# Optimization experiments

Measured on AMD Instinct MI355X. Metric: run time of the kernel, lower is better.

Reference implementation:

```python
import jax, jax.numpy as jnp
import numpy as np

B, N, DX, DZ = 4, 2048, 2, 128
PPD = (128, 128)
GRID_RANGE = ((-2.0, 2.0), (-2.0, 2.0))
INIT_LS = 0.1


def _construct_grid():
    axes = [jnp.linspace(lo, hi, p, dtype=jnp.float32) for (lo, hi), p in zip(GRID_RANGE, PPD)]
    mesh = jnp.meshgrid(*axes, indexing="ij")
    return jnp.stack(mesh, axis=-1)  # [128, 128, 2]


def setup_inputs() -> dict:
    key = jax.random.key(0)
    k1, k2 = jax.random.split(key)
    x = jax.random.uniform(k1, (B, N, DX), dtype=jnp.float32, minval=-2.0, maxval=2.0)
    z = jax.random.normal(k2, (B, N, DZ), dtype=jnp.float32)
    grid = _construct_grid()
    # inverse-softplus of init lengthscale, per dim
    ls0 = jnp.full((DX,), INIT_LS, dtype=jnp.float32)
    lengthscale_param = jnp.log(jnp.exp(ls0) - 1.0)
    return {"x": x, "z": z, "grid": grid, "lengthscale_param": lengthscale_param}


def reference(x, z, grid, lengthscale_param):
    b = x.shape[0]
    grid_shape = grid.shape[:-1]  # (128, 128)
    lengthscale = 1e-05 + jax.nn.softplus(lengthscale_param)  # [dx]
    grid_flat = grid.reshape(-1, grid.shape[-1])  # [M, dx], M = 16384
    # per-dim squared distance / l^2, summed over dx  -> [b, M, n]
    diff = grid_flat[None, :, None, :] - x[:, None, :, :]  # [b, M, n, dx]
    pre_exp = jnp.sum((diff * diff) / (lengthscale ** 2), axis=-1)
    weights = jnp.exp(-0.5 * pre_exp)  # [b, M, n]
    z_grid_flat = jnp.einsum("bmn,bnd->bmd", weights, z)  # [b, M, dz]
    z_grid = z_grid_flat.reshape((b,) + grid_shape + (z.shape[-1],))
    x_grid = jnp.broadcast_to(grid[None], (b,) + grid.shape)
    return (x_grid, z_grid)
```

## Files before the change

kernel.cpp:

```cpp
#include <hip/hip_runtime.h>

#define BATCH 4
#define NPTS  2048
#define DZDIM 128
#define GD    128
#define M_TOT (GD*GD)
#define TN    32
#define PW    40
#define PZ    40
#define ZP    2112
#define WBIN  15

typedef __attribute__((ext_vector_type(8))) __bf16 bf16x8;
typedef __attribute__((ext_vector_type(4))) float floatx4;

__device__ __forceinline__ unsigned int f2bf_bits(float x){
  unsigned int u = __float_as_uint(x);
  u += 0x7FFFu + ((u >> 16) & 1u);
  return u >> 16;
}
__device__ __forceinline__ int point_bin(float px){
  int bin = __float2int_rn((px + 2.0f) * (127.0f / 4.0f));
  return min(GD - 1, max(0, bin));
}

__global__ __launch_bounds__(256) void hist_xgrid_kernel(
    const float* __restrict__ x, const float* __restrict__ grid,
    float* __restrict__ out, int* __restrict__ binStart)
{
  const int tid = threadIdx.x;
  if (blockIdx.x < BATCH){
    __shared__ int h[GD];
    __shared__ int s[GD + 1];
    const int b = blockIdx.x;
    if (tid < GD) h[tid] = 0;
    __syncthreads();
    for (int n = tid; n < NPTS; n += 256)
      atomicAdd(&h[point_bin(x[(b*NPTS + n)*2])], 1);
    __syncthreads();
    if (tid == 0){
      int acc = 0;
#pragma unroll
      for (int j = 0; j < GD; ++j){ s[j] = acc; acc += h[j]; }
      s[GD] = acc;
    }
    __syncthreads();
    if (tid <= GD) binStart[b*(GD+1) + tid] = s[tid];
  } else {
    int idx = (blockIdx.x - BATCH) * 256 + tid;
    float g = grid[idx];
#pragma unroll
    for (int b = 0; b < BATCH; ++b) out[b*(GD*GD*2) + idx] = g;
  }
}

__global__ __launch_bounds__(256) void scatter_kernel(const float* __restrict__ x,
                                                      const int* __restrict__ binStart,
                                                      float2* __restrict__ xs,
                                                      int* __restrict__ perm){
  const int b = blockIdx.y;
  const int wv = threadIdx.x >> 6, lane = threadIdx.x & 63;
  const int bin = blockIdx.x * 4 + wv;
  int base = binStart[b*(GD+1) + bin];
  const float2* __restrict__ x2 = (const float2*)x;
  for (int n0 = 0; n0 < NPTS; n0 += 64){
    int n = n0 + lane;
    float2 xv = x2[b*NPTS + n];
    bool keep = (point_bin(xv.x) == bin);
    unsigned long long mask = __ballot(keep);
    int pre = __popcll(mask & ((1ull << lane) - 1ull));
    if (keep){
      xs[(long)b*ZP + base + pre] = xv;
      perm[b*NPTS + base + pre]   = n;
    }
    base += __popcll(mask);
  }
}

__global__ __launch_bounds__(256) void ztbuild_kernel(const float* __restrict__ z,
                                                      const int* __restrict__ perm,
                                                      unsigned short* __restrict__ zt){
  const int b  = blockIdx.y;
  const int j0 = blockIdx.x * 64;
  const int jj = threadIdx.x & 63;
  const int dq = threadIdx.x >> 6;
  const int j  = j0 + jj;
  const int n  = perm[b*NPTS + j];
  const float4* __restrict__ z4 = (const float4*)z;
  const long rb = (long)(b*NPTS + n) * 32;
#pragma unroll
  for (int r = 0; r < 8; ++r){
    int c = dq*8 + r;
    float4 v = z4[rb + c];
    long o = ((long)(b*DZDIM + 4*c) * ZP) + j;
    zt[o         ] = (unsigned short)f2bf_bits(v.x);
    zt[o +   ZP  ] = (unsigned short)f2bf_bits(v.y);
    zt[o + 2*ZP  ] = (unsigned short)f2bf_bits(v.z);
    zt[o + 3*ZP  ] = (unsigned short)f2bf_bits(v.w);
  }
}

__global__ __launch_bounds__(256, 4) void setconv_mfma_kernel(
    const float2* __restrict__ xs, const int* __restrict__ binStart,
    const unsigned short* __restrict__ zt, const float* __restrict__ lsp,
    float* __restrict__ outz)
{
  __shared__ __align__(16) unsigned short Wlds[2][64 * PW];
  __shared__ __align__(16) unsigned short Zlds[2][DZDIM * PZ];

  const int tid = threadIdx.x, lane = tid & 63, wv = tid >> 6;
  const int bid = blockIdx.x;
  const int g   = bid & 7;
  const int s   = bid >> 3;
  const int h   = s & 1;
  const int b   = (s >> 1) & 3;
  const int il  = s >> 3;
  const int i   = g*16 + il;
  const int my0 = h * 64;

  const float l0 = 1e-5f + log1pf(expf(lsp[0]));
  const float l1 = 1e-5f + log1pf(expf(lsp[1]));
  const float LOG2E = 1.4426950408889634f;
  const float c0 = -0.5f * LOG2E / (l0*l0);
  const float c1 = -0.5f * LOG2E / (l1*l1);
  const float step = 4.0f / 127.0f;
  const float gx   = -2.0f + (float)i * step;

  const int lo  = binStart[b*(GD+1) + max(0, i - WBIN)];
  const int hi  = binStart[b*(GD+1) + min(GD-1, i + WBIN) + 1];
  const int lo8 = lo & ~7;
  const int len = hi - lo8;
  const int T   = (len + TN - 1) / TN;

  const int   wnp = tid & 15;
  const int   mb  = tid >> 4;
  const float gy0 = -2.0f + (float)(my0 + mb) * step;

  int goff[3];
#pragma unroll
  for (int u = 0; u < 3; ++u){
    int gi = wv + 4*u;
    if (gi < 10){
      int pos = gi*64 + lane;
      int d = pos / 5, c = pos % 5;
      if (c > 3) c = 3;
      goff[u] = (b*DZDIM + d) * ZP + c*8;
    } else goff[u] = 0;
  }

  const int q  = lane >> 4;
  const int ml = lane & 15;

  floatx4 acc[8];
#pragma unroll
  for (int tz = 0; tz < 8; ++tz) acc[tz] = (floatx4){0.f, 0.f, 0.f, 0.f};

  auto stageZ = [&](int buf, int t){
    const int k0 = lo8 + t*TN;
#pragma unroll
    for (int u = 0; u < 3; ++u){
      int gi = wv + 4*u;
      if (gi < 10){
        const unsigned short* gp = zt + goff[u] + k0;
        __builtin_amdgcn_global_load_lds(
            (__attribute__((address_space(1))) void*)gp,
            (__attribute__((address_space(3))) void*)&Zlds[buf][gi*512],
            16, 0, 0);
      }
    }
  };
  auto stageW = [&](int buf, int t){
    const int ka = t*TN + 2*wnp;
    float4 xv = *(const float4*)&xs[(long)b*ZP + lo8 + ka];
    float d0a = gx - xv.x, d0b = gx - xv.z;
    float t0a = (ka     < len) ? c0*d0a*d0a : -1.0e30f;
    float t0b = (ka + 1 < len) ? c0*d0b*d0b : -1.0e30f;
#pragma unroll
    for (int r = 0; r < 4; ++r){
      float gy  = gy0 + (float)(16*r) * step;
      float dya = gy - xv.y, dyb = gy - xv.w;
      float ua = fmaf(c1*dya, dya, t0a);
      float ub = fmaf(c1*dyb, dyb, t0b);
      unsigned int v = f2bf_bits(__builtin_amdgcn_exp2f(ua))
                     | (f2bf_bits(__builtin_amdgcn_exp2f(ub)) << 16);
      *(unsigned int*)&Wlds[buf][(mb + 16*r)*PW + 2*wnp] = v;
    }
  };
  auto domfma = [&](int buf){
    bf16x8 af = *(const bf16x8*)&Wlds[buf][(wv*16 + ml)*PW + q*8];
#pragma unroll
    for (int tz = 0; tz < 8; ++tz){
      bf16x8 bf = *(const bf16x8*)&Zlds[buf][(tz*16 + ml)*PZ + q*8];
      acc[tz] = __builtin_amdgcn_mfma_f32_16x16x32_bf16(af, bf, acc[tz], 0, 0, 0);
    }
  };

  if (T > 0){
    stageZ(0, 0);
    stageW(0, 0);
    __syncthreads();
    for (int t = 0; t < T; ++t){
      const int cur = t & 1, nxt = 1 - cur;
      if (t + 1 < T) stageZ(nxt, t + 1);
      domfma(cur);
      if (t + 1 < T) stageW(nxt, t + 1);
      __syncthreads();
    }
  }

  const long obase = ((long)(b*M_TOT + i*GD + my0 + wv*16 + q*4) << 7) + ml;
#pragma unroll
  for (int tz = 0; tz < 8; ++tz)
#pragma unroll
    for (int r = 0; r < 4; ++r)
      outz[obase + ((long)r << 7) + tz*16] = acc[tz][r];
}

extern "C" void kernel_launch(void* const* d_in, const int* in_sizes, int n_in,
                              void* d_out, int out_size, void* d_ws, size_t ws_size,
                              hipStream_t stream)
{
  const float* x    = (const float*)d_in[0];
  const float* z    = (const float*)d_in[1];
  const float* grid = (const float*)d_in[2];
  const float* lsp  = (const float*)d_in[3];
  float* out = (float*)d_out;

  char* ws = (char*)d_ws;
  int*            binStart = (int*)ws;
  int*            perm     = (int*)(ws + 2064);
  float2*         xs       = (float2*)(ws + 2064 + 32768);
  unsigned short* zt       = (unsigned short*)(ws + 2064 + 32768 + 67584);

  hipLaunchKernelGGL(hist_xgrid_kernel, dim3(BATCH + GD), dim3(256), 0, stream,
                     x, grid, out, binStart);
  hipLaunchKernelGGL(scatter_kernel, dim3(GD/4, BATCH), dim3(256), 0, stream,
                     x, binStart, xs, perm);
  hipLaunchKernelGGL(ztbuild_kernel, dim3(NPTS/64, BATCH), dim3(256), 0, stream, z, perm, zt);
  hipLaunchKernelGGL(setconv_mfma_kernel, dim3(GD*2*BATCH), dim3(256), 0, stream,
                     xs, binStart, zt, lsp, out + BATCH*GD*GD*2);
}
```

Measured before the change: 111.4 us.

## Factor Gaussian weights into separable x/y parts and fuse prep kernels

The 2D Gaussian weight is split into a product of x and y factors. The y factors are precomputed per grid row and point into a global table (wy) by a combined z-transpose kernel. The x factors are computed per tile into a small shared buffer. The main MFMA kernel then builds its A fragments in registers by multiplying the two factors and packing them to bf16, which removes the per-tile exp evaluation and the shared-memory W staging. Histogram and scatter are also merged into one kernel using shared atomics, cutting a launch. The cost is extra global traffic for the wy table and a change in the order of points within each bin.

```diff
diff --git a/kernel.cpp b/kernel.cpp
--- a/kernel.cpp
+++ b/kernel.cpp
@@ -6,7 +6,6 @@
 #define GD    128
 #define M_TOT (GD*GD)
 #define TN    32
-#define PW    40
 #define PZ    40
 #define ZP    2112
 #define WBIN  15
@@ -24,19 +23,26 @@
   return min(GD - 1, max(0, bin));
 }
 
-__global__ __launch_bounds__(256) void hist_xgrid_kernel(
+__global__ __launch_bounds__(256) void prep_kernel(
     const float* __restrict__ x, const float* __restrict__ grid,
-    float* __restrict__ out, int* __restrict__ binStart)
+    float* __restrict__ out, int* __restrict__ binStart,
+    float2* __restrict__ xs, int* __restrict__ perm)
 {
   const int tid = threadIdx.x;
   if (blockIdx.x < BATCH){
     __shared__ int h[GD];
     __shared__ int s[GD + 1];
     const int b = blockIdx.x;
+    const float2* __restrict__ x2 = (const float2*)x;
     if (tid < GD) h[tid] = 0;
     __syncthreads();
-    for (int n = tid; n < NPTS; n += 256)
-      atomicAdd(&h[point_bin(x[(b*NPTS + n)*2])], 1);
+    float2 xv[8]; int bn[8];
+#pragma unroll
+    for (int u = 0; u < 8; ++u){
+      xv[u] = x2[b*NPTS + u*256 + tid];
+      bn[u] = point_bin(xv[u].x);
+      atomicAdd(&h[bn[u]], 1);
+    }
     __syncthreads();
     if (tid == 0){
       int acc = 0;
@@ -46,67 +52,71 @@
     }
     __syncthreads();
     if (tid <= GD) binStart[b*(GD+1) + tid] = s[tid];
+    if (tid < GD) h[tid] = 0;
+    __syncthreads();
+#pragma unroll
+    for (int u = 0; u < 8; ++u){
+      int j = s[bn[u]] + atomicAdd(&h[bn[u]], 1);
+      xs[(long)b*ZP + j]       = xv[u];
+      perm[b*NPTS + j]         = u*256 + tid;
+    }
   } else {
     int idx = (blockIdx.x - BATCH) * 256 + tid;
     float g = grid[idx];
 #pragma unroll
-    for (int b = 0; b < BATCH; ++b) out[b*(GD*GD*2) + idx] = g;
-  }
-}
-
-__global__ __launch_bounds__(256) void scatter_kernel(const float* __restrict__ x,
-                                                      const int* __restrict__ binStart,
-                                                      float2* __restrict__ xs,
-                                                      int* __restrict__ perm){
-  const int b = blockIdx.y;
-  const int wv = threadIdx.x >> 6, lane = threadIdx.x & 63;
-  const int bin = blockIdx.x * 4 + wv;
-  int base = binStart[b*(GD+1) + bin];
-  const float2* __restrict__ x2 = (const float2*)x;
-  for (int n0 = 0; n0 < NPTS; n0 += 64){
-    int n = n0 + lane;
-    float2 xv = x2[b*NPTS + n];
-    bool keep = (point_bin(xv.x) == bin);
-    unsigned long long mask = __ballot(keep);
-    int pre = __popcll(mask & ((1ull << lane) - 1ull));
-    if (keep){
-      xs[(long)b*ZP + base + pre] = xv;
-      perm[b*NPTS + base + pre]   = n;
-    }
-    base += __popcll(mask);
-  }
-}
-
-__global__ __launch_bounds__(256) void ztbuild_kernel(const float* __restrict__ z,
-                                                      const int* __restrict__ perm,
-                                                      unsigned short* __restrict__ zt){
-  const int b  = blockIdx.y;
-  const int j0 = blockIdx.x * 64;
-  const int jj = threadIdx.x & 63;
-  const int dq = threadIdx.x >> 6;
-  const int j  = j0 + jj;
-  const int n  = perm[b*NPTS + j];
+    for (int bb = 0; bb < BATCH; ++bb) out[bb*(GD*GD*2) + idx] = g;
+  }
+}
+
+__global__ __launch_bounds__(256) void ztwy_kernel(
+    const float* __restrict__ z, const float2* __restrict__ xs,
+    const int* __restrict__ perm, const float* __restrict__ lsp,
+    unsigned short* __restrict__ zt, float* __restrict__ wy)
+{
+  const int b   = blockIdx.y;
+  const int jj  = threadIdx.x & 31;
+  const int oct = threadIdx.x >> 5;
+  if (blockIdx.x >= NPTS/32){
+    int j = NPTS + (blockIdx.x - NPTS/32)*32 + jj;
+#pragma unroll
+    for (int yy = 0; yy < 16; ++yy)
+      wy[(long)(b*GD + oct*16 + yy)*ZP + j] = 0.f;
+    return;
+  }
+  const int j = blockIdx.x*32 + jj;
+  const int n = perm[b*NPTS + j];
   const float4* __restrict__ z4 = (const float4*)z;
   const long rb = (long)(b*NPTS + n) * 32;
 #pragma unroll
-  for (int r = 0; r < 8; ++r){
-    int c = dq*8 + r;
+  for (int r = 0; r < 4; ++r){
+    int c = oct*4 + r;
     float4 v = z4[rb + c];
     long o = ((long)(b*DZDIM + 4*c) * ZP) + j;
-    zt[o         ] = (unsigned short)f2bf_bits(v.x);
-    zt[o +   ZP  ] = (unsigned short)f2bf_bits(v.y);
-    zt[o + 2*ZP  ] = (unsigned short)f2bf_bits(v.z);
-    zt[o + 3*ZP  ] = (unsigned short)f2bf_bits(v.w);
+    zt[o        ] = (unsigned short)f2bf_bits(v.x);
+    zt[o +   ZP ] = (unsigned short)f2bf_bits(v.y);
+    zt[o + 2*ZP ] = (unsigned short)f2bf_bits(v.z);
+    zt[o + 3*ZP ] = (unsigned short)f2bf_bits(v.w);
+  }
+  const float l1 = 1e-5f + log1pf(expf(lsp[1]));
+  const float c1 = -0.5f * 1.4426950408889634f / (l1*l1);
+  const float step = 4.0f / 127.0f;
+  const float y = xs[(long)b*ZP + j].y;
+  float gy = -2.0f + (float)(oct*16) * step;
+#pragma unroll
+  for (int yy = 0; yy < 16; ++yy){
+    float d = gy - y;
+    wy[(long)(b*GD + oct*16 + yy)*ZP + j] = __builtin_amdgcn_exp2f(c1*d*d);
+    gy += step;
   }
 }
 
 __global__ __launch_bounds__(256, 4) void setconv_mfma_kernel(
     const float2* __restrict__ xs, const int* __restrict__ binStart,
-    const unsigned short* __restrict__ zt, const float* __restrict__ lsp,
-    float* __restrict__ outz)
-{
-  __shared__ __align__(16) unsigned short Wlds[2][64 * PW];
+    const unsigned short* __restrict__ zt, const float* __restrict__ wy,
+    const float* __restrict__ lsp, float* __restrict__ outz)
+{
   __shared__ __align__(16) unsigned short Zlds[2][DZDIM * PZ];
+  __shared__ __align__(16) float Wx[2][TN];
 
   const int tid = threadIdx.x, lane = tid & 63, wv = tid >> 6;
   const int bid = blockIdx.x;
@@ -119,10 +129,7 @@
   const int my0 = h * 64;
 
   const float l0 = 1e-5f + log1pf(expf(lsp[0]));
-  const float l1 = 1e-5f + log1pf(expf(lsp[1]));
-  const float LOG2E = 1.4426950408889634f;
-  const float c0 = -0.5f * LOG2E / (l0*l0);
-  const float c1 = -0.5f * LOG2E / (l1*l1);
+  const float c0 = -0.5f * 1.4426950408889634f / (l0*l0);
   const float step = 4.0f / 127.0f;
   const float gx   = -2.0f + (float)i * step;
 
@@ -131,10 +138,6 @@
   const int lo8 = lo & ~7;
   const int len = hi - lo8;
   const int T   = (len + TN - 1) / TN;
-
-  const int   wnp = tid & 15;
-  const int   mb  = tid >> 4;
-  const float gy0 = -2.0f + (float)(my0 + mb) * step;
 
   int goff[3];
 #pragma unroll
@@ -150,6 +153,7 @@
 
   const int q  = lane >> 4;
   const int ml = lane & 15;
+  const float* __restrict__ wyp = wy + (long)(b*GD + my0 + wv*16 + ml) * ZP + q*8;
 
   floatx4 acc[8];
 #pragma unroll
@@ -169,42 +173,45 @@
       }
     }
   };
-  auto stageW = [&](int buf, int t){
-    const int ka = t*TN + 2*wnp;
-    float4 xv = *(const float4*)&xs[(long)b*ZP + lo8 + ka];
-    float d0a = gx - xv.x, d0b = gx - xv.z;
-    float t0a = (ka     < len) ? c0*d0a*d0a : -1.0e30f;
-    float t0b = (ka + 1 < len) ? c0*d0b*d0b : -1.0e30f;
-#pragma unroll
-    for (int r = 0; r < 4; ++r){
-      float gy  = gy0 + (float)(16*r) * step;
-      float dya = gy - xv.y, dyb = gy - xv.w;
-      float ua = fmaf(c1*dya, dya, t0a);
-      float ub = fmaf(c1*dyb, dyb, t0b);
-      unsigned int v = f2bf_bits(__builtin_amdgcn_exp2f(ua))
-                     | (f2bf_bits(__builtin_amdgcn_exp2f(ub)) << 16);
-      *(unsigned int*)&Wlds[buf][(mb + 16*r)*PW + 2*wnp] = v;
-    }
-  };
-  auto domfma = [&](int buf){
-    bf16x8 af = *(const bf16x8*)&Wlds[buf][(wv*16 + ml)*PW + q*8];
-#pragma unroll
-    for (int tz = 0; tz < 8; ++tz){
-      bf16x8 bf = *(const bf16x8*)&Zlds[buf][(tz*16 + ml)*PZ + q*8];
-      acc[tz] = __builtin_amdgcn_mfma_f32_16x16x32_bf16(af, bf, acc[tz], 0, 0, 0);
+  auto stageWx = [&](int buf, int t){
+    if (tid < TN){
+      int ka = t*TN + tid;
+      float2 xv = xs[(long)b*ZP + lo8 + ka];
+      float d = gx - xv.x;
+      float w = __builtin_amdgcn_exp2f(c0*d*d);
+      Wx[buf][tid] = (ka < len) ? w : 0.f;
     }
   };
 
   if (T > 0){
     stageZ(0, 0);
-    stageW(0, 0);
+    stageWx(0, 0);
+    floatx4 wyA = *(const floatx4*)(wyp + lo8);
+    floatx4 wyB = *(const floatx4*)(wyp + lo8 + 4);
     __syncthreads();
     for (int t = 0; t < T; ++t){
       const int cur = t & 1, nxt = 1 - cur;
-      if (t + 1 < T) stageZ(nxt, t + 1);
-      domfma(cur);
-      if (t + 1 < T) stageW(nxt, t + 1);
+      if (t + 1 < T){ stageZ(nxt, t + 1); stageWx(nxt, t + 1); }
+      const int tp = (t + 1 < T) ? t + 1 : t;
+      floatx4 nA = *(const floatx4*)(wyp + lo8 + tp*TN);
+      floatx4 nB = *(const floatx4*)(wyp + lo8 + tp*TN + 4);
+      floatx4 wx0 = *(const floatx4*)&Wx[cur][q*8];
+      floatx4 wx1 = *(const floatx4*)&Wx[cur][q*8 + 4];
+      float p0 = wyA[0]*wx0[0], p1 = wyA[1]*wx0[1], p2 = wyA[2]*wx0[2], p3 = wyA[3]*wx0[3];
+      float p4 = wyB[0]*wx1[0], p5 = wyB[1]*wx1[1], p6 = wyB[2]*wx1[2], p7 = wyB[3]*wx1[3];
+      union { unsigned int u[4]; bf16x8 v; } A;
+      asm("v_cvt_pk_bf16_f32 %0, %1, %2" : "=v"(A.u[0]) : "v"(p0), "v"(p1));
+      asm("v_cvt_pk_bf16_f32 %0, %1, %2" : "=v"(A.u[1]) : "v"(p2), "v"(p3));
+      asm("v_cvt_pk_bf16_f32 %0, %1, %2" : "=v"(A.u[2]) : "v"(p4), "v"(p5));
+      asm("v_cvt_pk_bf16_f32 %0, %1, %2" : "=v"(A.u[3]) : "v"(p6), "v"(p7));
+      bf16x8 af = A.v;
+#pragma unroll
+      for (int tz = 0; tz < 8; ++tz){
+        bf16x8 bf = *(const bf16x8*)&Zlds[cur][(tz*16 + ml)*PZ + q*8];
+        acc[tz] = __builtin_amdgcn_mfma_f32_16x16x32_bf16(af, bf, acc[tz], 0, 0, 0);
+      }
       __syncthreads();
+      wyA = nA; wyB = nB;
     }
   }
 
@@ -229,14 +236,14 @@
   char* ws = (char*)d_ws;
   int*            binStart = (int*)ws;
   int*            perm     = (int*)(ws + 2064);
-  float2*         xs       = (float2*)(ws + 2064 + 32768);
-  unsigned short* zt       = (unsigned short*)(ws + 2064 + 32768 + 67584);
-
-  hipLaunchKernelGGL(hist_xgrid_kernel, dim3(BATCH + GD), dim3(256), 0, stream,
-                     x, grid, out, binStart);
-  hipLaunchKernelGGL(scatter_kernel, dim3(GD/4, BATCH), dim3(256), 0, stream,
-                     x, binStart, xs, perm);
-  hipLaunchKernelGGL(ztbuild_kernel, dim3(NPTS/64, BATCH), dim3(256), 0, stream, z, perm, zt);
+  float2*         xs       = (float2*)(ws + 34832);
+  unsigned short* zt       = (unsigned short*)(ws + 102416);
+  float*          wy       = (float*)(ws + 2265104);
+
+  hipLaunchKernelGGL(prep_kernel, dim3(BATCH + GD), dim3(256), 0, stream,
+                     x, grid, out, binStart, xs, perm);
+  hipLaunchKernelGGL(ztwy_kernel, dim3(NPTS/32 + 2, BATCH), dim3(256), 0, stream,
+                     z, xs, perm, lsp, zt, wy);
   hipLaunchKernelGGL(setconv_mfma_kernel, dim3(GD*2*BATCH), dim3(256), 0, stream,
-                     xs, binStart, zt, lsp, out + BATCH*GD*GD*2);
-}
+                     xs, binStart, zt, wy, lsp, out + BATCH*GD*GD*2);
+}
```

New measurement: 108.0 us. -3.0%, faster.
